# Kernel optimization log

Measured on AMD Instinct MI355X. Metric: run time of the kernel, lower is better.

Reference implementation:

```python
import jax, jax.numpy as jnp
import numpy as np

Nc, Nq = 100000, 20000
Fc, Fq = 300, 768
HID, H, L = 128, 4, 2
D = HID // H
OUT = 8
E = 400000
NT, ET = 2, 3


def setup_inputs() -> dict:
    key = jax.random.key(0)
    ks = jax.random.split(key, 24)
    def n(i, shape, s=1.0):
        return jax.random.normal(ks[i], shape, dtype=jnp.float32) * s
    return {
        'x_context': n(0, (Nc, Fc)),
        'x_question': n(1, (Nq, Fq)),
        'src_q2c': jax.random.randint(ks[2], (E,), 0, Nq),
        'dst_q2c': jax.random.randint(ks[3], (E,), 0, Nc),
        'src_c2c': jax.random.randint(ks[4], (E,), 0, Nc),
        'dst_c2c': jax.random.randint(ks[5], (E,), 0, Nc),
        'src_c2q': jax.random.randint(ks[6], (E,), 0, Nc),
        'dst_c2q': jax.random.randint(ks[7], (E,), 0, Nq),
        'in_W_context': n(8, (Fc, HID), 0.05),
        'in_b_context': jnp.zeros((HID,), jnp.float32),
        'in_W_question': n(9, (Fq, HID), 0.05),
        'in_b_question': jnp.zeros((HID,), jnp.float32),
        'k_W': n(10, (L, NT, HID, HID), 0.05),
        'k_b': jnp.zeros((L, NT, HID), jnp.float32),
        'q_W': n(11, (L, NT, HID, HID), 0.05),
        'q_b': jnp.zeros((L, NT, HID), jnp.float32),
        'v_W': n(12, (L, NT, HID, HID), 0.05),
        'v_b': jnp.zeros((L, NT, HID), jnp.float32),
        'a_W': n(13, (L, NT, HID, HID), 0.05),
        'a_b': jnp.zeros((L, NT, HID), jnp.float32),
        'skip': jnp.ones((L, NT), jnp.float32),
        'a_rel': n(14, (L, ET, H, D, D), 0.1),
        'm_rel': n(15, (L, ET, H, D, D), 0.1),
        'p_rel': jnp.ones((L, ET, H), jnp.float32),
        'out_W': n(16, (HID, OUT), 0.05),
        'out_b': jnp.zeros((OUT,), jnp.float32),
    }


def segment_softmax(logits, seg, num):
    # logits: [E, H], seg: [E] destination node ids
    m = jax.ops.segment_max(logits, seg, num_segments=num)
    m = jnp.where(jnp.isfinite(m), m, 0.0)
    e = jnp.exp(logits - m[seg])
    s = jax.ops.segment_sum(e, seg, num_segments=num)
    return e / (s[seg] + 1e-16)


def reference(x_context, x_question, src_q2c, dst_q2c, src_c2c, dst_c2c,
              src_c2q, dst_c2q, in_W_context, in_b_context, in_W_question,
              in_b_question, k_W, k_b, q_W, q_b, v_W, v_b, a_W, a_b, skip,
              a_rel, m_rel, p_rel, out_W, out_b):
    # node type 0 = 'context', 1 = 'question'
    x = [jax.nn.relu(x_context @ in_W_context + in_b_context),
         jax.nn.relu(x_question @ in_W_question + in_b_question)]
    Ns = [x[0].shape[0], x[1].shape[0]]
    # (src_nt, dst_nt, src_idx, dst_idx) per edge type
    edge_types = [(1, 0, src_q2c, dst_q2c),
                  (0, 0, src_c2c, dst_c2c),
                  (0, 1, src_c2q, dst_c2q)]
    scale = 1.0 / jnp.sqrt(jnp.float32(D))
    for l in range(L):
        k = [(x[nt] @ k_W[l, nt] + k_b[l, nt]).reshape(-1, H, D) for nt in range(NT)]
        q = [(x[nt] @ q_W[l, nt] + q_b[l, nt]).reshape(-1, H, D) for nt in range(NT)]
        v = [(x[nt] @ v_W[l, nt] + v_b[l, nt]).reshape(-1, H, D) for nt in range(NT)]
        agg = [jnp.zeros((Ns[nt], H, D), x[0].dtype) for nt in range(NT)]
        for et, (snt, dnt, src, dst) in enumerate(edge_types):
            k_rel = jnp.einsum('ehd,hdf->ehf', k[snt][src], a_rel[l, et])
            v_rel = jnp.einsum('ehd,hdf->ehf', v[snt][src], m_rel[l, et])
            logits = jnp.einsum('ehd,ehd->eh', q[dnt][dst], k_rel) * p_rel[l, et] * scale
            alpha = segment_softmax(logits, dst, Ns[dnt])  # [E, H]
            agg[dnt] = agg[dnt].at[dst].add(v_rel * alpha[:, :, None])
        for nt in range(NT):
            o = jax.nn.gelu(agg[nt].reshape(Ns[nt], HID), approximate=False)
            o = o @ a_W[l, nt] + a_b[l, nt]
            g = jax.nn.sigmoid(skip[l, nt])
            x[nt] = g * o + (1.0 - g) * x[nt]
    return x[0] @ out_W + out_b
```

## Files before the change

### kernel.cpp

```cpp
#include <hip/hip_runtime.h>

constexpr int NC = 100000;
constexpr int NQ = 20000;
constexpr int FC = 300;
constexpr int FQ = 768;
constexpr int NEDGE = 400000;
constexpr int NTOT = NC + NC + NQ;
constexpr int NTOT2 = NC + NQ;
constexpr int NB0 = (NC + 127) / 128;
constexpr int NB1 = (NQ + 127) / 128;
constexpr int NBALL = NB0 + NB1;
constexpr int NBC64 = (NC + 63) / 64;
constexpr int NBQ64 = (NQ + 63) / 64;
constexpr int NBALL64 = NBC64 + NBQ64;
constexpr float SCALE = 0.17677669529663687f;
constexpr float LOG2E = 1.4426950408889634f;

typedef __attribute__((ext_vector_type(8))) short bf16x8;
typedef __attribute__((ext_vector_type(4))) float f32x4;
typedef unsigned short u16;

__device__ __forceinline__ float gelu_f(float x) {
  return 0.5f * x * (1.0f + erff(x * 0.7071067811865476f));
}
__device__ __forceinline__ u16 bf16_rne(float x) {
  unsigned u = __float_as_uint(x);
  unsigned r = u + 0x7fffu + ((u >> 16) & 1u);
  return (u16)(r >> 16);
}
__device__ __forceinline__ float bf16_to_f(u16 h) {
  return __uint_as_float(((unsigned)h) << 16);
}
__device__ __forceinline__ void split2(float x, u16& hi, u16& lo) {
  hi = bf16_rne(x);
  lo = bf16_rne(x - bf16_to_f(hi));
}
__device__ __forceinline__ void splitT(float x, u16& hi, u16& lo) {
  hi = (u16)(__float_as_uint(x) >> 16);
  lo = bf16_rne(x - bf16_to_f(hi));
}

__global__ void k_count3(const int* __restrict__ d0, const int* __restrict__ d1,
                         const int* __restrict__ d2, int* __restrict__ counts) {
  int i = blockIdx.x * 256 + threadIdx.x;
  if (i >= 3 * NEDGE) return;
  int et = i / NEDGE, e = i - et * NEDGE;
  int d = (et == 0) ? d0[e] : (et == 1) ? d1[e] : d2[e];
  int base = (et == 0) ? 0 : (et == 1) ? NC : 2 * NC;
  atomicAdd(&counts[base + d], 1);
}

__global__ void k_scan_block(const int* __restrict__ in, int* __restrict__ out,
                             int* __restrict__ bsum, int n) {
  __shared__ int s[256];
  int tid = threadIdx.x;
  int i = blockIdx.x * 256 + tid;
  int v = (i < n) ? in[i] : 0;
  s[tid] = v;
  __syncthreads();
  for (int off = 1; off < 256; off <<= 1) {
    int t = (tid >= off) ? s[tid - off] : 0;
    __syncthreads();
    s[tid] += t;
    __syncthreads();
  }
  if (i < n) out[i] = s[tid] - v;
  if (tid == 255) bsum[blockIdx.x] = s[255];
}

__global__ void k_scan_sums(int* __restrict__ bsum, int nb) {
  __shared__ int s[1024];
  int tid = threadIdx.x;
  int v = (tid < nb) ? bsum[tid] : 0;
  s[tid] = v;
  __syncthreads();
  for (int off = 1; off < 1024; off <<= 1) {
    int t = (tid >= off) ? s[tid - off] : 0;
    __syncthreads();
    s[tid] += t;
    __syncthreads();
  }
  if (tid < nb) bsum[tid] = s[tid] - v;
}

__global__ void k_scan_add(int* __restrict__ ptr, const int* __restrict__ bsum,
                           int* __restrict__ cursor, int n, int total) {
  int i = blockIdx.x * 256 + threadIdx.x;
  if (i < n) {
    int v = ptr[i] + bsum[blockIdx.x];
    ptr[i] = v;
    cursor[i] = v;
  }
  if (i == 0) ptr[n] = total;
}

__global__ void k_scatter3(const int* __restrict__ s0, const int* __restrict__ s1,
                           const int* __restrict__ s2, const int* __restrict__ d0,
                           const int* __restrict__ d1, const int* __restrict__ d2,
                           int* __restrict__ cursor, int* __restrict__ srcs_out) {
  int i = blockIdx.x * 256 + threadIdx.x;
  if (i >= 3 * NEDGE) return;
  int et = i / NEDGE, e = i - et * NEDGE;
  int d = (et == 0) ? d0[e] : (et == 1) ? d1[e] : d2[e];
  int sv = (et == 0) ? s0[e] : (et == 1) ? s1[e] : s2[e];
  int base = (et == 0) ? 0 : (et == 1) ? NC : 2 * NC;
  int p = atomicAdd(&cursor[base + d], 1);
  srcs_out[p] = sv;
}

__global__ void prep_all(const float* __restrict__ kW, const float* __restrict__ kB,
                         const float* __restrict__ qW, const float* __restrict__ qB,
                         const float* __restrict__ vW, const float* __restrict__ vB,
                         const float* __restrict__ aW, const float* __restrict__ aB,
                         const float* __restrict__ arel, const float* __restrict__ mrel,
                         const float* __restrict__ prel,
                         u16* __restrict__ Bth, u16* __restrict__ Btl,
                         float* __restrict__ biasOut, int* __restrict__ counts) {
  int i = blockIdx.x;
  int col = threadIdx.x;
  int y = blockIdx.y;
  {
    int gid = (y * 128 + i) * 128 + col;
    if (gid < NTOT) counts[gid] = 0;
  }
  int l = y / 10, yy = y % 10;
  size_t lw = (size_t)l * 2 * 16384, lb = (size_t)l * 2 * 128;
  size_t le = (size_t)l * 3 * 4096, lp = (size_t)l * 3 * 4;
  const float *W = nullptr, *bb = nullptr, *rel = nullptr, *pr = nullptr;
  float mscale = 1.0f;
  bool fold = false;
  switch (yy) {
    case 0: W = qW + lw; bb = qB + lb; break;
    case 1: fold = true; W = kW + lw; bb = kB + lb; rel = arel + le + 4096; pr = prel + lp + 4; mscale = SCALE; break;
    case 2: fold = true; W = vW + lw; bb = vB + lb; rel = mrel + le + 4096; break;
    case 3: fold = true; W = kW + lw; bb = kB + lb; rel = arel + le + 8192; pr = prel + lp + 8; mscale = SCALE; break;
    case 4: fold = true; W = vW + lw; bb = vB + lb; rel = mrel + le + 8192; break;
    case 5: W = qW + lw + 16384; bb = qB + lb + 128; break;
    case 6: fold = true; W = kW + lw + 16384; bb = kB + lb + 128; rel = arel + le; pr = prel + lp; mscale = SCALE; break;
    case 7: fold = true; W = vW + lw + 16384; bb = vB + lb + 128; rel = mrel + le; break;
    case 8: W = aW + lw; bb = aB + lb; break;
    default: W = aW + lw + 16384; bb = aB + lb + 128; break;
  }
  int colOff = y * 128;
  if (!fold) {
    float v = W[i * 128 + col];
    u16 hi, lo;
    split2(v, hi, lo);
    Bth[(size_t)(colOff + col) * 128 + i] = hi;
    Btl[(size_t)(colOff + col) * 128 + i] = lo;
    if (i == 0) biasOut[colOff + col] = bb[col];
    return;
  }
  int h = col >> 5, f = col & 31;
  float m = (pr ? pr[h] : 1.0f) * mscale;
  float s = 0.0f;
  #pragma unroll
  for (int d = 0; d < 32; ++d)
    s += W[i * 128 + h * 32 + d] * rel[(h * 32 + d) * 32 + f];
  s *= m;
  u16 hi, lo;
  split2(s, hi, lo);
  Bth[(size_t)(colOff + col) * 128 + i] = hi;
  Btl[(size_t)(colOff + col) * 128 + i] = lo;
  if (i == 0) {
    float sb = 0.0f;
    #pragma unroll
    for (int d = 0; d < 32; ++d)
      sb += bb[h * 32 + d] * rel[(h * 32 + d) * 32 + f];
    biasOut[colOff + col] = sb * m;
  }
}

__global__ void split_in(const float* __restrict__ Wc, const float* __restrict__ bc,
                         const float* __restrict__ Wq, const float* __restrict__ bq,
                         u16* __restrict__ Bth, u16* __restrict__ Btl,
                         float* __restrict__ biasOut) {
  int n = blockIdx.x, y = blockIdx.y;
  const float* W = y ? Wq : Wc;
  const float* b = y ? bq : bc;
  int K = y ? FQ : FC, Kp = y ? 768 : 320;
  size_t boff = y ? (size_t)128 * 320 : 0;
  for (int k = threadIdx.x; k < Kp; k += 256) {
    float v = (k < K) ? W[(size_t)k * 128 + n] : 0.0f;
    u16 hi, lo;
    split2(v, hi, lo);
    Bth[boff + (size_t)n * Kp + k] = hi;
    Btl[boff + (size_t)n * Kp + k] = lo;
  }
  if (threadIdx.x == 0) biasOut[(y ? 128 : 0) + n] = b[n];
}

__global__ __launch_bounds__(256) void pipe_gemm(
    const float* __restrict__ Ac, const float* __restrict__ Aq,
    const u16* __restrict__ Bth, const u16* __restrict__ Btl,
    const float* __restrict__ biasBuf,
    u16* __restrict__ xh_all, u16* __restrict__ xl_all) {
  __shared__ u16 smem[15360];
  constexpr int AH = 0, AL = 2560, BH = 5120, BL = 10240;
  const int tid = threadIdx.x, lane = tid & 63, wv = tid >> 6;
  const int l15 = lane & 15, g4 = lane >> 4, koff = g4 * 8;
  const int srA = tid >> 2, scA = (tid & 3) * 8;
  const int srB = tid >> 1, scB = (tid & 1) * 16;

  const int bid = blockIdx.x;
  const int nt = (bid < NBC64) ? 0 : 1;
  const int m0 = nt ? (bid - NBC64) * 64 : bid * 64;
  const int M = nt ? NQ : NC;
  const int rowbase = nt ? NC : 0;
  const float* A32;
  int K, Kp, biasOff;
  size_t boff;
  if (nt == 0) { A32 = Ac; K = FC; Kp = 320; boff = 0; biasOff = 0; }
  else { A32 = Aq; K = FQ; Kp = 768; boff = (size_t)128 * 320; biasOff = 128; }
  size_t arow = (size_t)(m0 + srA) * K;
  const bool rowokA = (m0 + srA) < M;
  const int nk = (K + 31) / 32;

  f32x4 acc[8];
  #pragma unroll
  for (int ni = 0; ni < 8; ++ni) acc[ni] = (f32x4){0.f, 0.f, 0.f, 0.f};

  auto loadA = [&](float va[8], int k0) {
    if (rowokA && (k0 + 32 <= K)) {
      const float* ap = A32 + arow + k0 + scA;
      float4 f0 = *(const float4*)ap;
      float4 f1 = *(const float4*)(ap + 4);
      va[0] = f0.x; va[1] = f0.y; va[2] = f0.z; va[3] = f0.w;
      va[4] = f1.x; va[5] = f1.y; va[6] = f1.z; va[7] = f1.w;
    } else {
      #pragma unroll
      for (int j = 0; j < 8; ++j) {
        int kc = k0 + scA + j;
        va[j] = (rowokA && kc < K) ? A32[arow + kc] : 0.0f;
      }
    }
  };
  auto loadB = [&](uint4& bh0, uint4& bh1, uint4& bl0, uint4& bl1, int k0) {
    const u16* bp = Bth + boff + (size_t)srB * Kp + k0 + scB;
    bh0 = *(const uint4*)bp;
    bh1 = *(const uint4*)(bp + 8);
    const u16* lp = Btl + boff + (size_t)srB * Kp + k0 + scB;
    bl0 = *(const uint4*)lp;
    bl1 = *(const uint4*)(lp + 8);
  };

  float vaC[8], vaN[8], vaN2[8];
  uint4 bhC0, bhC1, blC0, blC1, bhN0, bhN1, blN0, blN1;
  loadA(vaC, 0);
  loadB(bhC0, bhC1, blC0, blC1, 0);
  if (nk > 1) loadA(vaN, 32);

  for (int ks = 0; ks < nk; ++ks) {
    {
      alignas(16) u16 hv[8], lv[8];
      #pragma unroll
      for (int j = 0; j < 8; ++j) splitT(vaC[j], hv[j], lv[j]);
      *(uint4*)&smem[AH + srA * 40 + scA] = *(const uint4*)hv;
      *(uint4*)&smem[AL + srA * 40 + scA] = *(const uint4*)lv;
      *(uint4*)&smem[BH + srB * 40 + scB] = bhC0;
      *(uint4*)&smem[BH + srB * 40 + scB + 8] = bhC1;
      *(uint4*)&smem[BL + srB * 40 + scB] = blC0;
      *(uint4*)&smem[BL + srB * 40 + scB + 8] = blC1;
    }
    __syncthreads();

    const bool moreA2 = (ks + 2) < nk;
    const bool moreB = (ks + 1) < nk;
    if (moreA2) loadA(vaN2, (ks + 2) * 32);
    if (moreB) loadB(bhN0, bhN1, blN0, blN1, (ks + 1) * 32);

    {
      int row = wv * 16 + l15;
      bf16x8 a_h = *(const bf16x8*)&smem[AH + row * 40 + koff];
      bf16x8 a_l = *(const bf16x8*)&smem[AL + row * 40 + koff];
      #pragma unroll
      for (int ni = 0; ni < 8; ++ni) {
        int col = ni * 16 + l15;
        bf16x8 b_h = *(const bf16x8*)&smem[BH + col * 40 + koff];
        bf16x8 b_l = *(const bf16x8*)&smem[BL + col * 40 + koff];
        acc[ni] = __builtin_amdgcn_mfma_f32_16x16x32_bf16(a_h, b_h, acc[ni], 0, 0, 0);
        acc[ni] = __builtin_amdgcn_mfma_f32_16x16x32_bf16(a_l, b_h, acc[ni], 0, 0, 0);
        acc[ni] = __builtin_amdgcn_mfma_f32_16x16x32_bf16(a_h, b_l, acc[ni], 0, 0, 0);
      }
    }
    __syncthreads();

    if (moreB) {
      #pragma unroll
      for (int j = 0; j < 8; ++j) vaC[j] = vaN[j];
      bhC0 = bhN0; bhC1 = bhN1; blC0 = blN0; blC1 = blN1;
    }
    if (moreA2) {
      #pragma unroll
      for (int j = 0; j < 8; ++j) vaN[j] = vaN2[j];
    }
  }

  const int rl0 = wv * 16 + g4 * 4;
  #pragma unroll
  for (int ni = 0; ni < 8; ++ni) {
    float bi = biasBuf[biasOff + ni * 16 + l15];
    #pragma unroll
    for (int rr = 0; rr < 4; ++rr)
      acc[ni][rr] = fmaxf(acc[ni][rr] + bi, 0.0f);
  }

  const int wrow = tid >> 2, wseg = tid & 3;
  #pragma unroll
  for (int ph = 0; ph < 2; ++ph) {
    if (ph) __syncthreads();
    #pragma unroll
    for (int ni = 0; ni < 8; ++ni) {
      #pragma unroll
      for (int rr = 0; rr < 4; ++rr) {
        u16 hh, ll;
        split2(acc[ni][rr], hh, ll);
        smem[(rl0 + rr) * 136 + ni * 16 + l15] = ph ? ll : hh;
      }
    }
    __syncthreads();
    int grow = m0 + wrow;
    if (grow < M) {
      u16* dstp = ph ? xl_all : xh_all;
      uint4* dst = (uint4*)&dstp[(size_t)(rowbase + grow) * 128 + wseg * 32];
      const uint4* src = (const uint4*)&smem[wrow * 136 + wseg * 32];
      #pragma unroll
      for (int j = 0; j < 4; ++j) dst[j] = src[j];
    }
  }
}

__global__ __launch_bounds__(256) void aproj_gemm(
    const u16* __restrict__ Ag,
    const u16* __restrict__ Bth, const u16* __restrict__ Btl,
    const float* __restrict__ biasBuf,
    u16* __restrict__ xh_all, u16* __restrict__ xl_all,
    const float* __restrict__ skip, int l) {
  __shared__ u16 smem[15360];
  constexpr int AH = 0, BHo = 5120, BLo = 10240;
  const int tid = threadIdx.x, lane = tid & 63, wv = tid >> 6;
  const int l15 = lane & 15, g4 = lane >> 4, koff = g4 * 8;
  const int sr = tid >> 1, sc = (tid & 1) * 16;

  const int bid = blockIdx.x;
  const int nt = (bid < NB0) ? 0 : 1;
  const int m0 = nt ? (bid - NB0) * 128 : bid * 128;
  const int M = nt ? NQ : NC;
  const int rowbase = nt ? NC : 0;
  const size_t boff = (size_t)(8 + nt) * 16384;
  const int biasOff = (8 + nt) * 128;
  const bool rowok = (m0 + sr) < M;

  f32x4 acc[2][8];
  #pragma unroll
  for (int mi = 0; mi < 2; ++mi)
    #pragma unroll
    for (int ni = 0; ni < 8; ++ni) acc[mi][ni] = (f32x4){0.f, 0.f, 0.f, 0.f};

  for (int k0 = 0; k0 < 128; k0 += 32) {
    uint4 h0 = {0, 0, 0, 0}, h1 = {0, 0, 0, 0};
    if (rowok) {
      const u16* ap = Ag + (size_t)(rowbase + m0 + sr) * 128 + k0 + sc;
      h0 = *(const uint4*)ap;
      h1 = *(const uint4*)(ap + 8);
    }
    *(uint4*)&smem[AH + sr * 40 + sc] = h0;
    *(uint4*)&smem[AH + sr * 40 + sc + 8] = h1;
    {
      const u16* bp = Bth + boff + (size_t)sr * 128 + k0 + sc;
      *(uint4*)&smem[BHo + sr * 40 + sc] = *(const uint4*)bp;
      *(uint4*)&smem[BHo + sr * 40 + sc + 8] = *(const uint4*)(bp + 8);
      const u16* lp = Btl + boff + (size_t)sr * 128 + k0 + sc;
      *(uint4*)&smem[BLo + sr * 40 + sc] = *(const uint4*)lp;
      *(uint4*)&smem[BLo + sr * 40 + sc + 8] = *(const uint4*)(lp + 8);
    }
    __syncthreads();

    bf16x8 a_h[2];
    #pragma unroll
    for (int mi = 0; mi < 2; ++mi) {
      int row = wv * 32 + mi * 16 + l15;
      a_h[mi] = *(const bf16x8*)&smem[AH + row * 40 + koff];
    }
    #pragma unroll
    for (int ni = 0; ni < 8; ++ni) {
      int col = ni * 16 + l15;
      bf16x8 b_h = *(const bf16x8*)&smem[BHo + col * 40 + koff];
      bf16x8 b_l = *(const bf16x8*)&smem[BLo + col * 40 + koff];
      #pragma unroll
      for (int mi = 0; mi < 2; ++mi) {
        acc[mi][ni] = __builtin_amdgcn_mfma_f32_16x16x32_bf16(a_h[mi], b_h, acc[mi][ni], 0, 0, 0);
        acc[mi][ni] = __builtin_amdgcn_mfma_f32_16x16x32_bf16(a_h[mi], b_l, acc[mi][ni], 0, 0, 0);
      }
    }
    __syncthreads();
  }

  float g = 1.0f / (1.0f + __expf(-skip[l * 2 + nt]));

  #pragma unroll
  for (int mi = 0; mi < 2; ++mi) {
    #pragma unroll
    for (int ni = 0; ni < 8; ++ni) {
      int colL = ni * 16 + l15;
      float bi = biasBuf[biasOff + colL];
      #pragma unroll
      for (int rr = 0; rr < 4; ++rr) {
        int row = m0 + wv * 32 + mi * 16 + g4 * 4 + rr;
        float o = acc[mi][ni][rr] + bi;
        if (row < M) {
          size_t idx = (size_t)(rowbase + row) * 128 + colL;
          float xo = bf16_to_f(xh_all[idx]) + bf16_to_f(xl_all[idx]);
          o = g * o + (1.0f - g) * xo;
        }
        acc[mi][ni][rr] = o;
      }
    }
  }

  const int wrow = tid >> 2, wseg = tid & 3;
  #pragma unroll
  for (int ph = 0; ph < 2; ++ph) {
    #pragma unroll
    for (int h = 0; h < 2; ++h) {
      if (ph || h) __syncthreads();
      if ((wv >> 1) == h) {
        #pragma unroll
        for (int mi = 0; mi < 2; ++mi) {
          int rl = (wv & 1) * 32 + mi * 16 + g4 * 4;
          #pragma unroll
          for (int ni = 0; ni < 8; ++ni) {
            #pragma unroll
            for (int rr = 0; rr < 4; ++rr) {
              u16 hh, ll;
              split2(acc[mi][ni][rr], hh, ll);
              smem[(rl + rr) * 136 + ni * 16 + l15] = ph ? ll : hh;
            }
          }
        }
      }
      __syncthreads();
      int grow = m0 + h * 64 + wrow;
      if (grow < M) {
        u16* dstp = ph ? xl_all : xh_all;
        uint4* dst = (uint4*)&dstp[(size_t)(rowbase + grow) * 128 + wseg * 32];
        const uint4* src = (const uint4*)&smem[wrow * 136 + wseg * 32];
        #pragma unroll
        for (int j = 0; j < 4; ++j) dst[j] = src[j];
      }
    }
  }
}

__global__ __launch_bounds__(256) void projN(
    const u16* __restrict__ xh_all,
    const u16* __restrict__ Bth, const float* __restrict__ biasBuf,
    u16* __restrict__ q_all, u16* __restrict__ kvA,
    u16* __restrict__ kvB1, u16* __restrict__ kvB2, int last) {
  __shared__ u16 smem[22528];
  constexpr int AH = 0, BH = 17408;
  const int tid = threadIdx.x, lane = tid & 63, wv = tid >> 6;
  const int l15 = lane & 15, g4 = lane >> 4, koff = g4 * 8;
  const int bid = blockIdx.x;
  const int nt = (bid < NB0) ? 0 : 1;
  const int m0 = nt ? (bid - NB0) * 128 : bid * 128;
  const int M = nt ? NQ : NC;
  const int abase = nt ? NC : 0;
  const int nslab = nt ? (last ? 2 : 3) : (last ? 3 : 5);

  {
    const int sr = tid >> 1, sc = (tid & 1) * 64;
    if ((m0 + sr) < M) {
      const u16* ap = xh_all + (size_t)(abase + m0 + sr) * 128 + sc;
      #pragma unroll
      for (int j = 0; j < 8; ++j)
        *(uint4*)&smem[AH + sr * 136 + sc + j * 8] = *(const uint4*)(ap + j * 8);
    } else {
      uint4 z = {0, 0, 0, 0};
      #pragma unroll
      for (int j = 0; j < 8; ++j)
        *(uint4*)&smem[AH + sr * 136 + sc + j * 8] = z;
    }
  }

  const int srB = tid >> 1, scB = (tid & 1) * 16;
  for (int s = 0; s < nslab; ++s) {
    int y = (nt == 1 && last) ? (s + 1) : s;
    int bslab = nt ? 5 + y : y;
    u16* cp; int ld, cb, crowbase;
    if (nt == 0) {
      switch (y) {
        case 0: cp = q_all; ld = 128; cb = 0; crowbase = 0; break;
        case 1: cp = kvB1; ld = 256; cb = 0; crowbase = 0; break;
        case 2: cp = kvB1; ld = 256; cb = 128; crowbase = 0; break;
        case 3: cp = kvB2; ld = 256; cb = 0; crowbase = 0; break;
        default: cp = kvB2; ld = 256; cb = 128; crowbase = 0; break;
      }
    } else {
      switch (y) {
        case 0: cp = q_all; ld = 128; cb = 0; crowbase = NC; break;
        case 1: cp = kvA; ld = 256; cb = 0; crowbase = 0; break;
        default: cp = kvA; ld = 256; cb = 128; crowbase = 0; break;
      }
    }

    f32x4 acc[2][8];
    #pragma unroll
    for (int mi = 0; mi < 2; ++mi)
      #pragma unroll
      for (int ni = 0; ni < 8; ++ni) acc[mi][ni] = (f32x4){0.f, 0.f, 0.f, 0.f};

    #pragma unroll
    for (int ks = 0; ks < 4; ++ks) {
      const u16* bp = Bth + (size_t)(bslab * 128 + srB) * 128 + ks * 32 + scB;
      uint4 b0 = *(const uint4*)bp;
      uint4 b1 = *(const uint4*)(bp + 8);
      __syncthreads();
      *(uint4*)&smem[BH + srB * 40 + scB] = b0;
      *(uint4*)&smem[BH + srB * 40 + scB + 8] = b1;
      __syncthreads();

      bf16x8 a_h[2];
      #pragma unroll
      for (int mi = 0; mi < 2; ++mi) {
        int row = wv * 32 + mi * 16 + l15;
        a_h[mi] = *(const bf16x8*)&smem[AH + row * 136 + ks * 32 + koff];
      }
      #pragma unroll
      for (int ni = 0; ni < 8; ++ni) {
        int col = ni * 16 + l15;
        bf16x8 b_h = *(const bf16x8*)&smem[BH + col * 40 + koff];
        #pragma unroll
        for (int mi = 0; mi < 2; ++mi)
          acc[mi][ni] = __builtin_amdgcn_mfma_f32_16x16x32_bf16(a_h[mi], b_h, acc[mi][ni], 0, 0, 0);
      }
    }

    #pragma unroll
    for (int h = 0; h < 4; ++h) {
      __syncthreads();
      if (wv == h) {
        #pragma unroll
        for (int mi = 0; mi < 2; ++mi) {
          int rl = mi * 16 + g4 * 4;
          #pragma unroll
          for (int ni = 0; ni < 8; ++ni) {
            float bi = biasBuf[bslab * 128 + ni * 16 + l15];
            #pragma unroll
            for (int rr = 0; rr < 4; ++rr)
              smem[BH + (rl + rr) * 136 + ni * 16 + l15] = bf16_rne(acc[mi][ni][rr] + bi);
          }
        }
      }
      __syncthreads();
      int r = tid >> 3, cseg = (tid & 7) * 16;
      int grow = m0 + h * 32 + r;
      if (grow < M) {
        uint4* dst = (uint4*)&cp[(size_t)(crowbase + grow) * ld + cb + cseg];
        const uint4* src = (const uint4*)&smem[BH + r * 136 + cseg];
        dst[0] = src[0];
        dst[1] = src[1];
      }
    }
  }
}

__device__ __forceinline__ void attn_seg(
    const u16* __restrict__ kv, int start, int end,
    const int* __restrict__ srcs, const float q8[8], int lane, float accO[8]) {
  if (start >= end) return;
  float sum = 0.0f;
  float acc[8];
  #pragma unroll
  for (int i = 0; i < 8; ++i) acc[i] = 0.0f;
  const int grp = lane >> 4;
  const int j = lane & 15;
  for (int e = start; e < end; e += 4) {
    int ee = e + grp;
    bool valid = ee < end;
    int cl = valid ? ee : end - 1;
    int s = srcs[cl];
    const u16* row = kv + (size_t)s * 256;
    uint4 uk = *(const uint4*)(row + j * 8);
    uint4 uv = *(const uint4*)(row + 128 + j * 8);
    float kr[8], vr[8];
    kr[0] = bf16_to_f((u16)(uk.x & 0xffffu)); kr[1] = bf16_to_f((u16)(uk.x >> 16));
    kr[2] = bf16_to_f((u16)(uk.y & 0xffffu)); kr[3] = bf16_to_f((u16)(uk.y >> 16));
    kr[4] = bf16_to_f((u16)(uk.z & 0xffffu)); kr[5] = bf16_to_f((u16)(uk.z >> 16));
    kr[6] = bf16_to_f((u16)(uk.w & 0xffffu)); kr[7] = bf16_to_f((u16)(uk.w >> 16));
    vr[0] = bf16_to_f((u16)(uv.x & 0xffffu)); vr[1] = bf16_to_f((u16)(uv.x >> 16));
    vr[2] = bf16_to_f((u16)(uv.y & 0xffffu)); vr[3] = bf16_to_f((u16)(uv.y >> 16));
    vr[4] = bf16_to_f((u16)(uv.z & 0xffffu)); vr[5] = bf16_to_f((u16)(uv.z >> 16));
    vr[6] = bf16_to_f((u16)(uv.w & 0xffffu)); vr[7] = bf16_to_f((u16)(uv.w >> 16));
    float p = q8[0] * kr[0];
    #pragma unroll
    for (int i = 1; i < 8; ++i) p = fmaf(q8[i], kr[i], p);
    p += __shfl_xor(p, 1);
    p += __shfl_xor(p, 2);
    p = fminf(p, 100.0f);
    float w = valid ? exp2f(p) : 0.0f;
    sum += w;
    #pragma unroll
    for (int i = 0; i < 8; ++i) acc[i] = fmaf(w, vr[i], acc[i]);
  }
  sum += __shfl_xor(sum, 16);
  sum += __shfl_xor(sum, 32);
  #pragma unroll
  for (int i = 0; i < 8; ++i) {
    acc[i] += __shfl_xor(acc[i], 16);
    acc[i] += __shfl_xor(acc[i], 32);
  }
  float inv = 1.0f / (sum + 1e-16f);
  #pragma unroll
  for (int i = 0; i < 8; ++i) accO[i] = fmaf(acc[i], inv, accO[i]);
}

__global__ __launch_bounds__(256) void attn_all(
    const u16* __restrict__ q_all, const u16* __restrict__ kvA,
    const u16* __restrict__ kvB1, const u16* __restrict__ kvB2,
    const int* __restrict__ ptr_all, const int* __restrict__ srcs_all,
    u16* __restrict__ agg_g, int ncap) {
  int wave = threadIdx.x >> 6, lane = threadIdx.x & 63;
  int node = blockIdx.x * 4 + wave;
  if (node >= ncap) return;
  int j = lane & 15;
  float q8[8];
  {
    uint4 u = *(const uint4*)&q_all[(size_t)node * 128 + j * 8];
    q8[0] = bf16_to_f((u16)(u.x & 0xffffu)) * LOG2E; q8[1] = bf16_to_f((u16)(u.x >> 16)) * LOG2E;
    q8[2] = bf16_to_f((u16)(u.y & 0xffffu)) * LOG2E; q8[3] = bf16_to_f((u16)(u.y >> 16)) * LOG2E;
    q8[4] = bf16_to_f((u16)(u.z & 0xffffu)) * LOG2E; q8[5] = bf16_to_f((u16)(u.z >> 16)) * LOG2E;
    q8[6] = bf16_to_f((u16)(u.w & 0xffffu)) * LOG2E; q8[7] = bf16_to_f((u16)(u.w >> 16)) * LOG2E;
  }
  float accO[8];
  #pragma unroll
  for (int i = 0; i < 8; ++i) accO[i] = 0.0f;
  if (node < NC) {
    attn_seg(kvA, ptr_all[node], ptr_all[node + 1], srcs_all, q8, lane, accO);
    attn_seg(kvB1, ptr_all[NC + node], ptr_all[NC + node + 1], srcs_all, q8, lane, accO);
  } else {
    int idx = 2 * NC + (node - NC);
    attn_seg(kvB2, ptr_all[idx], ptr_all[idx + 1], srcs_all, q8, lane, accO);
  }
  if (lane < 16) {
    alignas(16) u16 hv[8];
    #pragma unroll
    for (int i = 0; i < 8; ++i) hv[i] = bf16_rne(gelu_f(accO[i]));
    *(uint4*)&agg_g[(size_t)node * 128 + j * 8] = *(const uint4*)hv;
  }
}

__global__ __launch_bounds__(256) void gemm_out(const u16* __restrict__ Xh,
                                                const u16* __restrict__ Xl,
                                                const float* __restrict__ W,
                                                const float* __restrict__ b,
                                                float* __restrict__ out, int M) {
  __shared__ float Ws[1024];
  __shared__ float As[32][129];
  int tid = threadIdx.x;
  int m0 = blockIdx.x * 32;
  *(float4*)&Ws[tid * 4] = *(const float4*)&W[tid * 4];
  {
    int r = tid >> 3;
    int c0 = (tid & 7) * 16;
    if (m0 + r < M) {
      const u16* hp = Xh + (size_t)(m0 + r) * 128 + c0;
      const u16* lp = Xl + (size_t)(m0 + r) * 128 + c0;
      #pragma unroll
      for (int j = 0; j < 16; ++j) As[r][c0 + j] = bf16_to_f(hp[j]) + bf16_to_f(lp[j]);
    } else {
      #pragma unroll
      for (int j = 0; j < 16; ++j) As[r][c0 + j] = 0.0f;
    }
  }
  __syncthreads();
  int r = tid >> 3, c = tid & 7;
  float sum = b[c];
  #pragma unroll 16
  for (int k = 0; k < 128; ++k) sum = fmaf(As[r][k], Ws[k * 8 + c], sum);
  if (m0 + r < M) out[(size_t)(m0 + r) * 8 + c] = sum;
}

static inline size_t align256(size_t x) { return (x + 255) & ~(size_t)255; }

extern "C" void kernel_launch(void* const* d_in, const int* in_sizes, int n_in,
                              void* d_out, int out_size, void* d_ws, size_t ws_size,
                              hipStream_t stream) {
  const float* x_context = (const float*)d_in[0];
  const float* x_question = (const float*)d_in[1];
  const int* src_q2c = (const int*)d_in[2];
  const int* dst_q2c = (const int*)d_in[3];
  const int* src_c2c = (const int*)d_in[4];
  const int* dst_c2c = (const int*)d_in[5];
  const int* src_c2q = (const int*)d_in[6];
  const int* dst_c2q = (const int*)d_in[7];
  const float* inWc = (const float*)d_in[8];
  const float* inbc = (const float*)d_in[9];
  const float* inWq = (const float*)d_in[10];
  const float* inbq = (const float*)d_in[11];
  const float* kW = (const float*)d_in[12];
  const float* kB = (const float*)d_in[13];
  const float* qW = (const float*)d_in[14];
  const float* qB = (const float*)d_in[15];
  const float* vW = (const float*)d_in[16];
  const float* vB = (const float*)d_in[17];
  const float* aW = (const float*)d_in[18];
  const float* aB = (const float*)d_in[19];
  const float* skip = (const float*)d_in[20];
  const float* arel = (const float*)d_in[21];
  const float* mrel = (const float*)d_in[22];
  const float* prel = (const float*)d_in[23];
  const float* outW = (const float*)d_in[24];
  const float* outb = (const float*)d_in[25];

  char* base = (char*)d_ws;
  size_t off = 0;
  auto carve = [&](size_t bytes) -> void* {
    void* p = base + off;
    off = align256(off + bytes);
    return p;
  };
  u16* xh_all = (u16*)carve((size_t)NTOT2 * 128 * 2);
  u16* xl_all = (u16*)carve((size_t)NTOT2 * 128 * 2);
  u16* q_all = (u16*)carve((size_t)NTOT2 * 128 * 2);
  u16* kvA = (u16*)carve((size_t)NQ * 256 * 2);
  u16* kvB1 = (u16*)carve((size_t)NC * 256 * 2);
  u16* kvB2 = (u16*)carve((size_t)NC * 256 * 2);
  u16* agg_g = (u16*)carve((size_t)NTOT2 * 128 * 2);
  u16* Bth = (u16*)carve((size_t)2560 * 128 * 2);
  u16* Btl = (u16*)carve((size_t)2560 * 128 * 2);
  u16* BthI = (u16*)carve((size_t)(320 + 768) * 128 * 2);
  u16* BtlI = (u16*)carve((size_t)(320 + 768) * 128 * 2);
  float* biasBuf = (float*)carve(2560 * 4);
  float* biasIn = (float*)carve(256 * 4);
  int* ptr_all = (int*)carve((size_t)(NTOT + 1) * 4);
  int* srcs_all = (int*)carve((size_t)3 * NEDGE * 4);
  int* counts = (int*)carve((size_t)NTOT * 4);
  int* cursor = (int*)carve((size_t)NTOT * 4);
  int* blksums = (int*)carve(2048 * 4);

  split_in<<<dim3(128, 2), 256, 0, stream>>>(inWc, inbc, inWq, inbq, BthI, BtlI, biasIn);
  prep_all<<<dim3(128, 20), 128, 0, stream>>>(kW, kB, qW, qB, vW, vB, aW, aB,
                                              arel, mrel, prel, Bth, Btl, biasBuf, counts);

  {
    int nb = (NTOT + 255) / 256;
    k_count3<<<(3 * NEDGE + 255) / 256, 256, 0, stream>>>(dst_q2c, dst_c2c, dst_c2q, counts);
    k_scan_block<<<nb, 256, 0, stream>>>(counts, ptr_all, blksums, NTOT);
    k_scan_sums<<<1, 1024, 0, stream>>>(blksums, nb);
    k_scan_add<<<nb, 256, 0, stream>>>(ptr_all, blksums, cursor, NTOT, 3 * NEDGE);
    k_scatter3<<<(3 * NEDGE + 255) / 256, 256, 0, stream>>>(
        src_q2c, src_c2c, src_c2q, dst_q2c, dst_c2c, dst_c2q, cursor, srcs_all);
  }

  pipe_gemm<<<NBALL64, 256, 0, stream>>>(x_context, x_question, BthI, BtlI, biasIn,
                                         xh_all, xl_all);

  for (int l = 0; l < 2; ++l) {
    const int last = (l == 1);
    const u16* BthL = Bth + (size_t)l * 10 * 128 * 128;
    const u16* BtlL = Btl + (size_t)l * 10 * 128 * 128;
    const float* biasL = biasBuf + (size_t)l * 1280;
    projN<<<NBALL, 256, 0, stream>>>(xh_all, BthL, biasL, q_all, kvA, kvB1, kvB2, last);
    int ncap = last ? NC : NTOT2;
    attn_all<<<(ncap + 3) / 4, 256, 0, stream>>>(q_all, kvA, kvB1, kvB2,
                                                 ptr_all, srcs_all, agg_g, ncap);
    aproj_gemm<<<last ? NB0 : NBALL, 256, 0, stream>>>(agg_g, BthL, BtlL, biasL,
                                                       xh_all, xl_all, skip, l);
  }

  gemm_out<<<(NC + 31) / 32, 256, 0, stream>>>(xh_all, xl_all, outW, outb, (float*)d_out, NC);
}
```

Baseline: 698.2 us.

## Fold CSR count and scatter kernels into weight-prep and input GEMM launches

After: 707.3 us. About the same (+1.3%).

```diff
diff --git a/kernel.cpp b/kernel.cpp
--- a/kernel.cpp
+++ b/kernel.cpp
@@ -13,6 +13,7 @@
 constexpr int NBC64 = (NC + 63) / 64;
 constexpr int NBQ64 = (NQ + 63) / 64;
 constexpr int NBALL64 = NBC64 + NBQ64;
+constexpr int NSCAT = (3 * NEDGE + 255) / 256;
 constexpr float SCALE = 0.17677669529663687f;
 constexpr float LOG2E = 1.4426950408889634f;
 
@@ -38,16 +39,6 @@
 __device__ __forceinline__ void splitT(float x, u16& hi, u16& lo) {
   hi = (u16)(__float_as_uint(x) >> 16);
   lo = bf16_rne(x - bf16_to_f(hi));
-}
-
-__global__ void k_count3(const int* __restrict__ d0, const int* __restrict__ d1,
-                         const int* __restrict__ d2, int* __restrict__ counts) {
-  int i = blockIdx.x * 256 + threadIdx.x;
-  if (i >= 3 * NEDGE) return;
-  int et = i / NEDGE, e = i - et * NEDGE;
-  int d = (et == 0) ? d0[e] : (et == 1) ? d1[e] : d2[e];
-  int base = (et == 0) ? 0 : (et == 1) ? NC : 2 * NC;
-  atomicAdd(&counts[base + d], 1);
 }
 
 __global__ void k_scan_block(const int* __restrict__ in, int* __restrict__ out,
@@ -94,20 +85,6 @@
   if (i == 0) ptr[n] = total;
 }
 
-__global__ void k_scatter3(const int* __restrict__ s0, const int* __restrict__ s1,
-                           const int* __restrict__ s2, const int* __restrict__ d0,
-                           const int* __restrict__ d1, const int* __restrict__ d2,
-                           int* __restrict__ cursor, int* __restrict__ srcs_out) {
-  int i = blockIdx.x * 256 + threadIdx.x;
-  if (i >= 3 * NEDGE) return;
-  int et = i / NEDGE, e = i - et * NEDGE;
-  int d = (et == 0) ? d0[e] : (et == 1) ? d1[e] : d2[e];
-  int sv = (et == 0) ? s0[e] : (et == 1) ? s1[e] : s2[e];
-  int base = (et == 0) ? 0 : (et == 1) ? NC : 2 * NC;
-  int p = atomicAdd(&cursor[base + d], 1);
-  srcs_out[p] = sv;
-}
-
 __global__ void prep_all(const float* __restrict__ kW, const float* __restrict__ kB,
                          const float* __restrict__ qW, const float* __restrict__ qB,
                          const float* __restrict__ vW, const float* __restrict__ vB,
@@ -115,13 +92,21 @@
                          const float* __restrict__ arel, const float* __restrict__ mrel,
                          const float* __restrict__ prel,
                          u16* __restrict__ Bth, u16* __restrict__ Btl,
-                         float* __restrict__ biasOut, int* __restrict__ counts) {
+                         float* __restrict__ biasOut,
+                         const int* __restrict__ d0, const int* __restrict__ d1,
+                         const int* __restrict__ d2, int* __restrict__ counts) {
   int i = blockIdx.x;
   int col = threadIdx.x;
   int y = blockIdx.y;
   {
-    int gid = (y * 128 + i) * 128 + col;
-    if (gid < NTOT) counts[gid] = 0;
+    const int nth = 20 * 128 * 128;
+    int gtid = (y * 128 + i) * 128 + col;
+    for (int e = gtid; e < 3 * NEDGE; e += nth) {
+      int et = e / NEDGE, ee = e - et * NEDGE;
+      int d = (et == 0) ? d0[ee] : (et == 1) ? d1[ee] : d2[ee];
+      int base = (et == 0) ? 0 : (et == 1) ? NC : 2 * NC;
+      atomicAdd(&counts[base + d], 1);
+    }
   }
   int l = y / 10, yy = y % 10;
   size_t lw = (size_t)l * 2 * 16384, lb = (size_t)l * 2 * 128;
@@ -174,8 +159,13 @@
 __global__ void split_in(const float* __restrict__ Wc, const float* __restrict__ bc,
                          const float* __restrict__ Wq, const float* __restrict__ bq,
                          u16* __restrict__ Bth, u16* __restrict__ Btl,
-                         float* __restrict__ biasOut) {
+                         float* __restrict__ biasOut, int* __restrict__ counts) {
   int n = blockIdx.x, y = blockIdx.y;
+  {
+    const int nth = 2 * 128 * 256;
+    int gtid = (y * 128 + n) * 256 + threadIdx.x;
+    for (int i = gtid; i < NTOT; i += nth) counts[i] = 0;
+  }
   const float* W = y ? Wq : Wc;
   const float* b = y ? bq : bc;
   int K = y ? FQ : FC, Kp = y ? 768 : 320;
@@ -194,15 +184,33 @@
     const float* __restrict__ Ac, const float* __restrict__ Aq,
     const u16* __restrict__ Bth, const u16* __restrict__ Btl,
     const float* __restrict__ biasBuf,
-    u16* __restrict__ xh_all, u16* __restrict__ xl_all) {
+    u16* __restrict__ xh_all, u16* __restrict__ xl_all,
+    const int* __restrict__ s0, const int* __restrict__ s1, const int* __restrict__ s2,
+    const int* __restrict__ d0, const int* __restrict__ d1, const int* __restrict__ d2,
+    int* __restrict__ cursor, int* __restrict__ srcs_out) {
   __shared__ u16 smem[15360];
   constexpr int AH = 0, AL = 2560, BH = 5120, BL = 10240;
-  const int tid = threadIdx.x, lane = tid & 63, wv = tid >> 6;
+  const int tid = threadIdx.x;
+
+  if (blockIdx.x < NSCAT) {
+    int i = blockIdx.x * 256 + tid;
+    if (i < 3 * NEDGE) {
+      int et = i / NEDGE, e = i - et * NEDGE;
+      int d = (et == 0) ? d0[e] : (et == 1) ? d1[e] : d2[e];
+      int sv = (et == 0) ? s0[e] : (et == 1) ? s1[e] : s2[e];
+      int base = (et == 0) ? 0 : (et == 1) ? NC : 2 * NC;
+      int p = atomicAdd(&cursor[base + d], 1);
+      srcs_out[p] = sv;
+    }
+    return;
+  }
+
+  const int lane = tid & 63, wv = tid >> 6;
   const int l15 = lane & 15, g4 = lane >> 4, koff = g4 * 8;
   const int srA = tid >> 2, scA = (tid & 3) * 8;
   const int srB = tid >> 1, scB = (tid & 1) * 16;
 
-  const int bid = blockIdx.x;
+  const int bid = blockIdx.x - NSCAT;
   const int nt = (bid < NBC64) ? 0 : 1;
   const int m0 = nt ? (bid - NBC64) * 64 : bid * 64;
   const int M = nt ? NQ : NC;
@@ -739,22 +747,21 @@
   int* cursor = (int*)carve((size_t)NTOT * 4);
   int* blksums = (int*)carve(2048 * 4);
 
-  split_in<<<dim3(128, 2), 256, 0, stream>>>(inWc, inbc, inWq, inbq, BthI, BtlI, biasIn);
+  split_in<<<dim3(128, 2), 256, 0, stream>>>(inWc, inbc, inWq, inbq, BthI, BtlI, biasIn, counts);
   prep_all<<<dim3(128, 20), 128, 0, stream>>>(kW, kB, qW, qB, vW, vB, aW, aB,
-                                              arel, mrel, prel, Bth, Btl, biasBuf, counts);
+                                              arel, mrel, prel, Bth, Btl, biasBuf,
+                                              dst_q2c, dst_c2c, dst_c2q, counts);
 
   {
     int nb = (NTOT + 255) / 256;
-    k_count3<<<(3 * NEDGE + 255) / 256, 256, 0, stream>>>(dst_q2c, dst_c2c, dst_c2q, counts);
     k_scan_block<<<nb, 256, 0, stream>>>(counts, ptr_all, blksums, NTOT);
     k_scan_sums<<<1, 1024, 0, stream>>>(blksums, nb);
     k_scan_add<<<nb, 256, 0, stream>>>(ptr_all, blksums, cursor, NTOT, 3 * NEDGE);
-    k_scatter3<<<(3 * NEDGE + 255) / 256, 256, 0, stream>>>(
-        src_q2c, src_c2c, src_c2q, dst_q2c, dst_c2c, dst_c2q, cursor, srcs_all);
-  }
-
-  pipe_gemm<<<NBALL64, 256, 0, stream>>>(x_context, x_question, BthI, BtlI, biasIn,
-                                         xh_all, xl_all);
+  }
+
+  pipe_gemm<<<NSCAT + NBALL64, 256, 0, stream>>>(
+      x_context, x_question, BthI, BtlI, biasIn, xh_all, xl_all,
+      src_q2c, src_c2c, src_c2q, dst_q2c, dst_c2c, dst_c2q, cursor, srcs_all);
 
   for (int l = 0; l < 2; ++l) {
     const int last = (l == 1);
```
